# Kernel tuning notes

Measured on AMD Instinct MI355X. Metric: run time of the kernel, lower is better.

## Reference

```python
import jax, jax.numpy as jnp
import numpy as np

H_OUT, W_OUT = 48, 320


def setup_inputs() -> dict:
    key = jax.random.key(0)
    k1, k2, k3 = jax.random.split(key, 3)
    x = jax.random.normal(k1, (8, 64, 200, 320), dtype=jnp.float32)
    bboxes = jax.random.randint(k2, (256, 4), 0, 320, dtype=jnp.int32)
    box_img = jax.random.randint(k3, (256,), 0, 8, dtype=jnp.int32)
    return {"x": x, "bboxes": bboxes, "box_img": box_img}


def reference(x, bboxes, box_img):
    # x: [B, C, H, W]; bboxes: [N, 4] int (x0, y0, x1, y1); box_img: [N] image index
    B, C, H, W = x.shape
    x0 = jnp.clip(bboxes[:, 0], 0, W - 1)
    y0 = jnp.clip(bboxes[:, 1], 0, H - 1)
    x1 = jnp.clip(bboxes[:, 2], 0, W - 1)
    y1 = jnp.clip(bboxes[:, 3], 0, H - 1)
    x1 = jnp.maximum(x1, x0)
    y1 = jnp.maximum(y1, y0)
    # inclusive crop: height/width of each crop
    h = y1 - y0 + 1  # [N]
    w = x1 - x0 + 1  # [N]
    # F.interpolate default mode='nearest': src = floor(dst * in/out)
    i = jnp.arange(H_OUT, dtype=jnp.int32)
    j = jnp.arange(W_OUT, dtype=jnp.int32)
    rows = y0[:, None] + (i[None, :] * h[:, None]) // H_OUT  # [N, H_OUT]
    cols = x0[:, None] + (j[None, :] * w[:, None]) // W_OUT  # [N, W_OUT]
    # single fused gather: advanced indices broadcast to [N, H_OUT, W_OUT],
    # with the ':' channel slice moved to the last axis -> [N, H_OUT, W_OUT, C]
    g = x[box_img[:, None, None], :, rows[:, :, None], cols[:, None, :]]
    return jnp.transpose(g, (0, 3, 1, 2))  # [N, C, H_OUT, W_OUT]
```

## Files before the change

kernel.cpp:

```cpp
#include <hip/hip_runtime.h>

#define C_CH   64
#define H_IN   200
#define W_IN   320
#define H_OUT  48
#define W_OUT  320
#define N_BOX  256

typedef float float4v __attribute__((ext_vector_type(4), aligned(16)));

__global__ __launch_bounds__(320, 2) void roi_crop_kernel(
    const float* __restrict__ x,
    const int*   __restrict__ bboxes,
    const int*   __restrict__ box_img,
    float*       __restrict__ out)
{
    __shared__ float tile[H_OUT * W_OUT];

    const int c   = blockIdx.x;
    const int box = blockIdx.y;
    const int t   = threadIdx.x;

    int x0 = bboxes[box * 4 + 0];
    int y0 = bboxes[box * 4 + 1];
    int x1 = bboxes[box * 4 + 2];
    int y1 = bboxes[box * 4 + 3];

    x0 = min(max(x0, 0), W_IN - 1);
    y0 = min(max(y0, 0), H_IN - 1);
    x1 = min(max(x1, 0), W_IN - 1);
    y1 = min(max(y1, 0), H_IN - 1);
    x1 = max(x1, x0);
    y1 = max(y1, y0);

    const int h = y1 - y0 + 1;
    const int w = x1 - x0 + 1;
    const int img = box_img[box];

    const float* __restrict__ plane_in =
        x + ((size_t)img * C_CH + c) * (H_IN * W_IN);
    float* __restrict__ plane_out =
        out + ((size_t)box * C_CH + c) * (H_OUT * W_OUT);

    float4v v[12];
    #pragma unroll
    for (int k = 0; k < 12; ++k) {
        const int p   = t + k * 320;
        const int i   = p / 80;
        const int wrd = p % 80;
        const int r   = y0 + (i * h) / H_OUT;
        v[k] = *(const float4v*)(plane_in + (size_t)r * W_IN + wrd * 4);
    }
    #pragma unroll
    for (int k = 0; k < 12; ++k) {
        const int p = t + k * 320;
        *(float4v*)&tile[p * 4] = v[k];
    }
    __syncthreads();

    const int col = x0 + (t * w) / W_OUT;
    #pragma unroll 8
    for (int i = 0; i < H_OUT; ++i) {
        const float val = tile[i * W_OUT + col];
        __builtin_nontemporal_store(val, plane_out + i * W_OUT + t);
    }
}

extern "C" void kernel_launch(void* const* d_in, const int* in_sizes, int n_in,
                              void* d_out, int out_size, void* d_ws, size_t ws_size,
                              hipStream_t stream) {
    const float* x       = (const float*)d_in[0];
    const int*   bboxes  = (const int*)d_in[1];
    const int*   box_img = (const int*)d_in[2];
    float*       out     = (float*)d_out;

    dim3 grid(C_CH, N_BOX);
    dim3 block(320);
    roi_crop_kernel<<<grid, block, 0, stream>>>(x, bboxes, box_img, out);
}
```

Before: 1.053 ms.

## Load only the bbox column span and unique source rows into shared tile

Instead of staging 48 full-width input rows per plane, the kernel now loads only the float4 words covering the box's column range, and for short boxes only the h distinct source rows, using a magic-number reciprocal to split the flat index into row and word. The gather stage remaps output rows to the deduplicated tile rows and uses a compact row stride. This cuts global read traffic for narrow or short boxes, at the cost of divergent guarded loads and more index arithmetic. The launch-bounds occupancy hint is also dropped.

```diff
diff --git a/kernel.cpp b/kernel.cpp
--- a/kernel.cpp
+++ b/kernel.cpp
@@ -1,4 +1,5 @@
 #include <hip/hip_runtime.h>
+#include <stdint.h>
 
 #define C_CH   64
 #define H_IN   200
@@ -9,32 +10,28 @@
 
 typedef float float4v __attribute__((ext_vector_type(4), aligned(16)));
 
-__global__ __launch_bounds__(320, 2) void roi_crop_kernel(
+__global__ __launch_bounds__(320) void roi_crop_kernel(
     const float* __restrict__ x,
     const int*   __restrict__ bboxes,
     const int*   __restrict__ box_img,
     float*       __restrict__ out)
 {
-    __shared__ float tile[H_OUT * W_OUT];
+    __shared__ __align__(16) float tile[H_OUT * W_OUT];
 
     const int c   = blockIdx.x;
     const int box = blockIdx.y;
     const int t   = threadIdx.x;
 
-    int x0 = bboxes[box * 4 + 0];
-    int y0 = bboxes[box * 4 + 1];
-    int x1 = bboxes[box * 4 + 2];
-    int y1 = bboxes[box * 4 + 3];
-
-    x0 = min(max(x0, 0), W_IN - 1);
-    y0 = min(max(y0, 0), H_IN - 1);
-    x1 = min(max(x1, 0), W_IN - 1);
-    y1 = min(max(y1, 0), H_IN - 1);
+    const int4 bb = *(const int4*)(bboxes + box * 4);
+    int x0 = min(max(bb.x, 0), W_IN - 1);
+    int y0 = min(max(bb.y, 0), H_IN - 1);
+    int x1 = min(max(bb.z, 0), W_IN - 1);
+    int y1 = min(max(bb.w, 0), H_IN - 1);
     x1 = max(x1, x0);
     y1 = max(y1, y0);
 
-    const int h = y1 - y0 + 1;
-    const int w = x1 - x0 + 1;
+    const int h   = y1 - y0 + 1;
+    const int w   = x1 - x0 + 1;
     const int img = box_img[box];
 
     const float* __restrict__ plane_in =
@@ -42,26 +39,42 @@
     float* __restrict__ plane_out =
         out + ((size_t)box * C_CH + c) * (H_OUT * W_OUT);
 
+    const int  x0f4    = x0 >> 2;
+    const int  K4      = (x1 >> 2) - x0f4 + 1;
+    const int  x0f     = x0f4 << 2;
+    const bool small_h = (h <= H_OUT);
+    const int  nur     = small_h ? h : H_OUT;
+    const uint32_t total = (uint32_t)(nur * K4);
+
+    const uint32_t inv = (K4 > 1)
+        ? (uint32_t)((0x100000000ULL + (uint32_t)K4 - 1) / (uint32_t)K4) : 0u;
+
     float4v v[12];
     #pragma unroll
     for (int k = 0; k < 12; ++k) {
-        const int p   = t + k * 320;
-        const int i   = p / 80;
-        const int wrd = p % 80;
-        const int r   = y0 + (i * h) / H_OUT;
-        v[k] = *(const float4v*)(plane_in + (size_t)r * W_IN + wrd * 4);
+        const uint32_t p = (uint32_t)t + (uint32_t)k * 320u;
+        if (p < total) {
+            const uint32_t row = (K4 == 1) ? p : __umulhi(p, inv);
+            const uint32_t wrd = p - row * (uint32_t)K4;
+            const int r = small_h ? (y0 + (int)row)
+                                  : (y0 + ((int)row * h) / H_OUT);
+            v[k] = *(const float4v*)(plane_in + (size_t)r * W_IN + x0f + (wrd << 2));
+        }
     }
     #pragma unroll
     for (int k = 0; k < 12; ++k) {
-        const int p = t + k * 320;
-        *(float4v*)&tile[p * 4] = v[k];
+        const uint32_t p = (uint32_t)t + (uint32_t)k * 320u;
+        if (p < total)
+            *(float4v*)&tile[p << 2] = v[k];
     }
     __syncthreads();
 
-    const int col = x0 + (t * w) / W_OUT;
+    const int ldrow = K4 << 2;
+    const int cadj  = (x0 + (t * w) / W_OUT) - x0f;
     #pragma unroll 8
     for (int i = 0; i < H_OUT; ++i) {
-        const float val = tile[i * W_OUT + col];
+        const int s   = small_h ? (i * h) / H_OUT : i;
+        const float val = tile[s * ldrow + cadj];
         __builtin_nontemporal_store(val, plane_out + i * W_OUT + t);
     }
 }
```

After: 1.078 ms. 2.4% more time.
